# Performance work log

Measured on AMD Instinct MI355X. Metric: run time of the kernel, lower is better.

## Reference

```python
import jax, jax.numpy as jnp
import numpy as np

B, S, DM, H = 4, 4096, 1024, 16
HD = DM // H

def setup_inputs() -> dict:
    key = jax.random.key(0)
    ks = jax.random.split(key, 9)
    sc = 1.0 / np.sqrt(DM)
    return {
        "x": jax.random.normal(ks[0], (B, S, DM), dtype=jnp.float32),
        "Wq": jax.random.normal(ks[1], (DM, DM), dtype=jnp.float32) * sc,
        "bq": jnp.zeros((DM,), dtype=jnp.float32),
        "Wk": jax.random.normal(ks[2], (DM, DM), dtype=jnp.float32) * sc,
        "bk": jnp.zeros((DM,), dtype=jnp.float32),
        "Wv": jax.random.normal(ks[3], (DM, DM), dtype=jnp.float32) * sc,
        "bv": jnp.zeros((DM,), dtype=jnp.float32),
        "Wo": jax.random.normal(ks[4], (DM, DM), dtype=jnp.float32) * sc,
        "bo": jnp.zeros((DM,), dtype=jnp.float32),
    }

def _heads(t):
    # [B,S,DM] -> [B,H,S,HD]
    return t.reshape(B, S, H, HD).transpose(0, 2, 1, 3)

def reference(x, Wq, bq, Wk, bk, Wv, bv, Wo, bo):
    q = _heads(x @ Wq.T + bq)
    k = _heads(x @ Wk.T + bk)
    v = _heads(x @ Wv.T + bv)
    q = jax.nn.elu(q) + 1.0  # positive feature map
    k = jax.nn.elu(k) + 1.0
    # kv aggregation: [B,H,HD,HD]
    kv = jnp.einsum('bhsd,bhse->bhde', k, v)
    qkv = jnp.einsum('bhsd,bhde->bhse', q, kv)  # [B,H,S,HD]
    k_sum = k.sum(axis=2)  # [B,H,HD]
    normalizer = jnp.einsum('bhsd,bhd->bhs', q, k_sum) + 1e-6
    out = qkv / normalizer[..., None]
    out = out.transpose(0, 2, 1, 3).reshape(B, S, DM)
    return out @ Wo.T + bo  # dropout is identity in eval
```

## Files before the change

### kernel.cpp

```cpp
#include <hip/hip_runtime.h>
#include <math.h>

#define NROWS  16384
#define DMODEL 1024
#define NHEAD  16
#define HDIM   64
#define SEQ    4096
#define NBATCH 4
#define NBH    64
#define SCHUNK 16
#define M1     1048576u

typedef __attribute__((ext_vector_type(8))) short bf16x8;
typedef __attribute__((ext_vector_type(4))) float f32x4;

__device__ __forceinline__ unsigned short f2bf(float f) {
    unsigned u = __float_as_uint(f);
    u += 0x7FFFu + ((u >> 16) & 1u);
    return (unsigned short)(u >> 16);
}
__device__ __forceinline__ float bf2f(unsigned short h) {
    return __uint_as_float((unsigned)h << 16);
}

__device__ __forceinline__ void gload16(const void* g, void* l) {
    __builtin_amdgcn_global_load_lds(
        (const __attribute__((address_space(1))) unsigned int*)g,
        (__attribute__((address_space(3))) unsigned int*)l, 16, 0, 0);
}

__global__ __launch_bounds__(256)
void split_pair(const float* __restrict__ a, unsigned short* __restrict__ hi,
                unsigned short* __restrict__ lo, int n4)
{
    int i = blockIdx.x * 256 + threadIdx.x;
    const int stride = gridDim.x * 256;
    for (; i < n4; i += stride) {
        const float4 v = ((const float4*)a)[i];
        ushort4 H, L;
        H.x = f2bf(v.x); L.x = f2bf(v.x - bf2f(H.x));
        H.y = f2bf(v.y); L.y = f2bf(v.y - bf2f(H.y));
        H.z = f2bf(v.z); L.z = f2bf(v.z - bf2f(H.z));
        H.w = f2bf(v.w); L.w = f2bf(v.w - bf2f(H.w));
        ((ushort4*)hi)[i] = H;
        ((ushort4*)lo)[i] = L;
    }
}

__global__ __launch_bounds__(256)
void split_w4(const float* __restrict__ a0, const float* __restrict__ a1,
              const float* __restrict__ a2, const float* __restrict__ a3,
              unsigned short* __restrict__ dst)
{
    const int y = blockIdx.y;
    const float* src = (y == 0) ? a0 : (y == 1) ? a1 : (y == 2) ? a2 : a3;
    unsigned short* hi = dst + (size_t)y * 2u * M1;
    unsigned short* lo = hi + M1;
    const int i = blockIdx.x * 256 + threadIdx.x;
    const float4 v = ((const float4*)src)[i];
    ushort4 H, L;
    H.x = f2bf(v.x); L.x = f2bf(v.x - bf2f(H.x));
    H.y = f2bf(v.y); L.y = f2bf(v.y - bf2f(H.y));
    H.z = f2bf(v.z); L.z = f2bf(v.z - bf2f(H.z));
    H.w = f2bf(v.w); L.w = f2bf(v.w - bf2f(H.w));
    ((ushort4*)hi)[i] = H;
    ((ushort4*)lo)[i] = L;
}

template<int ELU>
__global__ __launch_bounds__(256)
void gemm_split(const unsigned short* __restrict__ Ah, const unsigned short* __restrict__ Al,
                const unsigned short* __restrict__ Wh, const unsigned short* __restrict__ Wl,
                const float* __restrict__ bias, float* __restrict__ C)
{
    __shared__ unsigned short lds[4 * 4096];
    const int t    = threadIdx.x;
    const int lane = t & 63;
    const int w    = t >> 6;
    const int wr   = w >> 1;
    const int wc   = w & 1;
    const int m0   = blockIdx.x * 128;
    const int n0   = blockIdx.y * 128;
    const int srow = lane >> 2;
    const int scol = (lane & 3) * 8;
    const int fr   = lane & 15;
    const int kq   = (lane >> 4) * 8;

    f32x4 acc[4][4];
#pragma unroll
    for (int i = 0; i < 4; ++i)
#pragma unroll
        for (int j = 0; j < 4; ++j)
#pragma unroll
            for (int e = 0; e < 4; ++e) acc[i][j][e] = 0.f;

    for (int k0 = 0; k0 < DMODEL; k0 += 32) {
#pragma unroll
        for (int c = 0; c < 2; ++c) {
            const int rr = (c * 4 + w) * 16 + srow;
            const size_t goffA = (size_t)(m0 + rr) * DMODEL + k0 + scol;
            const size_t goffB = (size_t)(n0 + rr) * DMODEL + k0 + scol;
            unsigned short* lbase = (unsigned short*)lds + (c * 4 + w) * 512;
            gload16(Ah + goffA, lbase);
            gload16(Al + goffA, lbase + 4096);
            gload16(Wh + goffB, lbase + 8192);
            gload16(Wl + goffB, lbase + 12288);
        }
        __syncthreads();

        bf16x8 ah[4], al[4], bh[4], bl[4];
#pragma unroll
        for (int i = 0; i < 4; ++i) {
            const int ar = wr * 64 + i * 16 + fr;
            const int br = wc * 64 + i * 16 + fr;
            ah[i] = *(const bf16x8*)&lds[ar * 32 + kq];
            al[i] = *(const bf16x8*)&lds[4096 + ar * 32 + kq];
            bh[i] = *(const bf16x8*)&lds[8192 + br * 32 + kq];
            bl[i] = *(const bf16x8*)&lds[12288 + br * 32 + kq];
        }
#pragma unroll
        for (int i = 0; i < 4; ++i)
#pragma unroll
            for (int j = 0; j < 4; ++j) {
                acc[i][j] = __builtin_amdgcn_mfma_f32_16x16x32_bf16(ah[i], bh[j], acc[i][j], 0, 0, 0);
                acc[i][j] = __builtin_amdgcn_mfma_f32_16x16x32_bf16(ah[i], bl[j], acc[i][j], 0, 0, 0);
                acc[i][j] = __builtin_amdgcn_mfma_f32_16x16x32_bf16(al[i], bh[j], acc[i][j], 0, 0, 0);
            }
        __syncthreads();
    }

    const int crow0 = m0 + wr * 64 + (lane >> 4) * 4;
    const int ccol0 = n0 + wc * 64 + fr;
#pragma unroll
    for (int j = 0; j < 4; ++j) {
        const int col = ccol0 + j * 16;
        const float bv = bias[col];
#pragma unroll
        for (int i = 0; i < 4; ++i) {
            const int row = crow0 + i * 16;
#pragma unroll
            for (int r = 0; r < 4; ++r) {
                float v = acc[i][j][r] + bv;
                if (ELU) v = (v > 0.f) ? (v + 1.f) : __expf(v);
                C[(size_t)(row + r) * DMODEL + col] = v;
            }
        }
    }
}

__global__ __launch_bounds__(512)
void kv_partial(const float* __restrict__ k, const float* __restrict__ v,
                float* __restrict__ kvp, float* __restrict__ ksp)
{
    __shared__ float Ks[32][64];
    __shared__ float Vs[32][64];
    const int t  = threadIdx.x;
    const int bh = blockIdx.x;
    const int b  = bh >> 4;
    const int h  = bh & 15;
    const int sc = blockIdx.y;
    const int d  = t & 63;
    const int e0 = (t >> 6) * 8;

    float acc[8];
#pragma unroll
    for (int j = 0; j < 8; ++j) acc[j] = 0.f;
    float ks = 0.f;

    const size_t rowbase = (size_t)b * SEQ;
    const int sbeg = sc * (SEQ / SCHUNK);
    const int send = sbeg + (SEQ / SCHUNK);
    const int lrow = t >> 4;
    const int lc4  = (t & 15) * 4;

    for (int s0 = sbeg; s0 < send; s0 += 32) {
        const size_t g = (rowbase + s0 + lrow) * DMODEL + h * HDIM + lc4;
        *(float4*)&Ks[lrow][lc4] = *(const float4*)&k[g];
        *(float4*)&Vs[lrow][lc4] = *(const float4*)&v[g];
        __syncthreads();
#pragma unroll 8
        for (int sp = 0; sp < 32; ++sp) {
            const float kd = Ks[sp][d];
            if (t < 64) ks += Ks[sp][t];
            const float4 v0 = *(const float4*)&Vs[sp][e0 + 0];
            const float4 v1 = *(const float4*)&Vs[sp][e0 + 4];
            acc[0] = fmaf(kd, v0.x, acc[0]);  acc[1] = fmaf(kd, v0.y, acc[1]);
            acc[2] = fmaf(kd, v0.z, acc[2]);  acc[3] = fmaf(kd, v0.w, acc[3]);
            acc[4] = fmaf(kd, v1.x, acc[4]);  acc[5] = fmaf(kd, v1.y, acc[5]);
            acc[6] = fmaf(kd, v1.z, acc[6]);  acc[7] = fmaf(kd, v1.w, acc[7]);
        }
        __syncthreads();
    }

    const size_t base = ((size_t)sc * NBH + bh) * HDIM;
    float4 o0; o0.x = acc[0]; o0.y = acc[1]; o0.z = acc[2]; o0.w = acc[3];
    float4 o1; o1.x = acc[4]; o1.y = acc[5]; o1.z = acc[6]; o1.w = acc[7];
    *(float4*)&kvp[(base + d) * HDIM + e0 + 0] = o0;
    *(float4*)&kvp[(base + d) * HDIM + e0 + 4] = o1;
    if (t < 64) ksp[base + t] = ks;
}

__global__ __launch_bounds__(256)
void kv_reduce(const float* __restrict__ kvp, const float* __restrict__ ksp,
               float* __restrict__ kv, float* __restrict__ ksum)
{
    const int i = blockIdx.x * 256 + threadIdx.x;
    const int NKV = NBH * HDIM * HDIM;
    if (i < NKV) {
        float s = 0.f;
#pragma unroll
        for (int c = 0; c < SCHUNK; ++c) s += kvp[(size_t)c * NKV + i];
        kv[i] = s;
    }
    if (i < NBH * HDIM) {
        float s = 0.f;
#pragma unroll
        for (int c = 0; c < SCHUNK; ++c) s += ksp[(size_t)c * NBH * HDIM + i];
        ksum[i] = s;
    }
}

__global__ __launch_bounds__(256)
void qkv_norm(const float* __restrict__ q, const float* __restrict__ kv,
              const float* __restrict__ ksum,
              unsigned short* __restrict__ ah, unsigned short* __restrict__ al)
{
    __shared__ float Qs[64][68];
    __shared__ float KVs[64][64];
    __shared__ float kss[64];
    const int t  = threadIdx.x;
    const int s0 = blockIdx.x * 64;
    const int b  = blockIdx.y;
    const int h  = blockIdx.z;
    const int bh = b * NHEAD + h;

#pragma unroll
    for (int i = 0; i < 4; ++i) {
        const int idx = i * 256 + t;
        const int row = idx >> 4;
        const int c4  = (idx & 15) * 4;
        const float4 vq = *(const float4*)&q[((size_t)b * SEQ + s0 + row) * DMODEL + h * HDIM + c4];
        *(float4*)&Qs[row][c4] = vq;
        *(float4*)&((float*)KVs)[idx * 4] = *(const float4*)&kv[(size_t)bh * HDIM * HDIM + idx * 4];
    }
    if (t < 64) kss[t] = ksum[(size_t)bh * HDIM + t];
    __syncthreads();

    const int r  = t >> 2;
    const int e0 = (t & 3) * 16;
    float out[16];
#pragma unroll
    for (int j = 0; j < 16; ++j) out[j] = 0.f;
    float nrm = 0.f;

#pragma unroll 8
    for (int d = 0; d < 64; ++d) {
        const float qd = Qs[r][d];
        nrm = fmaf(qd, kss[d], nrm);
        const float4 k0 = *(const float4*)&KVs[d][e0 + 0];
        const float4 k1 = *(const float4*)&KVs[d][e0 + 4];
        const float4 k2 = *(const float4*)&KVs[d][e0 + 8];
        const float4 k3 = *(const float4*)&KVs[d][e0 + 12];
        out[0]  = fmaf(qd, k0.x, out[0]);  out[1]  = fmaf(qd, k0.y, out[1]);
        out[2]  = fmaf(qd, k0.z, out[2]);  out[3]  = fmaf(qd, k0.w, out[3]);
        out[4]  = fmaf(qd, k1.x, out[4]);  out[5]  = fmaf(qd, k1.y, out[5]);
        out[6]  = fmaf(qd, k1.z, out[6]);  out[7]  = fmaf(qd, k1.w, out[7]);
        out[8]  = fmaf(qd, k2.x, out[8]);  out[9]  = fmaf(qd, k2.y, out[9]);
        out[10] = fmaf(qd, k2.z, out[10]); out[11] = fmaf(qd, k2.w, out[11]);
        out[12] = fmaf(qd, k3.x, out[12]); out[13] = fmaf(qd, k3.y, out[13]);
        out[14] = fmaf(qd, k3.z, out[14]); out[15] = fmaf(qd, k3.w, out[15]);
    }

    const float inv = 1.f / (nrm + 1e-6f);
    const size_t gbase = ((size_t)b * SEQ + s0 + r) * DMODEL + h * HDIM + e0;
#pragma unroll
    for (int g4 = 0; g4 < 4; ++g4) {
        ushort4 H, L;
        const float v0 = out[g4*4+0] * inv;
        const float v1 = out[g4*4+1] * inv;
        const float v2 = out[g4*4+2] * inv;
        const float v3 = out[g4*4+3] * inv;
        H.x = f2bf(v0); L.x = f2bf(v0 - bf2f(H.x));
        H.y = f2bf(v1); L.y = f2bf(v1 - bf2f(H.y));
        H.z = f2bf(v2); L.z = f2bf(v2 - bf2f(H.z));
        H.w = f2bf(v3); L.w = f2bf(v3 - bf2f(H.w));
        *(ushort4*)&ah[gbase + g4 * 4] = H;
        *(ushort4*)&al[gbase + g4 * 4] = L;
    }
}

extern "C" void kernel_launch(void* const* d_in, const int* in_sizes, int n_in,
                              void* d_out, int out_size, void* d_ws, size_t ws_size,
                              hipStream_t stream)
{
    const float* x  = (const float*)d_in[0];
    const float* Wq = (const float*)d_in[1];
    const float* bq = (const float*)d_in[2];
    const float* Wk = (const float*)d_in[3];
    const float* bk = (const float*)d_in[4];
    const float* Wv = (const float*)d_in[5];
    const float* bv = (const float*)d_in[6];
    const float* Wo = (const float*)d_in[7];
    const float* bo = (const float*)d_in[8];

    unsigned short* xh = (unsigned short*)d_ws;
    unsigned short* xl = xh + (size_t)NROWS * DMODEL;
    unsigned short* wsp = xl + (size_t)NROWS * DMODEL;
    float* buf0 = (float*)(wsp + 8u * M1);
    float* kv   = buf0 + (size_t)NROWS * DMODEL;
    float* ksum = kv + NBH * HDIM * HDIM;
    float* kvp  = ksum + NBH * HDIM;
    float* ksp  = kvp + (size_t)SCHUNK * NBH * HDIM * HDIM;
    float* vbuf = (float*)d_out;

    const dim3 gg(NROWS / 128, DMODEL / 128);
    const int n4x = NROWS * DMODEL / 4;

    split_w4<<<dim3(1024, 4), 256, 0, stream>>>(Wq, Wk, Wv, Wo, wsp);
    split_pair<<<4096, 256, 0, stream>>>(x, xh, xl, n4x);
    gemm_split<1><<<gg, 256, 0, stream>>>(xh, xl, wsp + 2u * M1, wsp + 3u * M1, bk, buf0);
    gemm_split<0><<<gg, 256, 0, stream>>>(xh, xl, wsp + 4u * M1, wsp + 5u * M1, bv, vbuf);
    kv_partial<<<dim3(NBH, SCHUNK), 512, 0, stream>>>(buf0, vbuf, kvp, ksp);
    kv_reduce<<<1024, 256, 0, stream>>>(kvp, ksp, kv, ksum);
    gemm_split<1><<<gg, 256, 0, stream>>>(xh, xl, wsp, wsp + M1, bq, buf0);
    qkv_norm<<<dim3(SEQ / 64, NBATCH, NHEAD), 256, 0, stream>>>(buf0, kv, ksum, xh, xl);
    gemm_split<0><<<gg, 256, 0, stream>>>(xh, xl, wsp + 6u * M1, wsp + 7u * M1, bo, (float*)d_out);
}
```

Before: 582.1 us.

## Use 256x256 double-buffered split-bf16 GEMM with 8 waves and block swizzle

Replaces the 128x128 single-buffered split-bf16 GEMM with a 256x256-tile, 512-thread kernel. Each block keeps two LDS stages so global loads for the next K step overlap MFMA work on the current one, and the stage loads are interleaved per A-phase with s_barrier and setprio hints. A block-index swizzle groups blocks that share A rows to improve L2 reuse. The larger tile doubles per-wave accumulators (128 fp32 regs), which raises register pressure and gives only 256 blocks, which may leave CUs underfilled.

```diff
diff --git a/kernel.cpp b/kernel.cpp
--- a/kernel.cpp
+++ b/kernel.cpp
@@ -68,75 +68,100 @@
 }
 
 template<int ELU>
-__global__ __launch_bounds__(256)
-void gemm_split(const unsigned short* __restrict__ Ah, const unsigned short* __restrict__ Al,
-                const unsigned short* __restrict__ Wh, const unsigned short* __restrict__ Wl,
-                const float* __restrict__ bias, float* __restrict__ C)
-{
-    __shared__ unsigned short lds[4 * 4096];
+__global__ __launch_bounds__(512)
+void gemm_split8(const unsigned short* __restrict__ Ah, const unsigned short* __restrict__ Al,
+                 const unsigned short* __restrict__ Wh, const unsigned short* __restrict__ Wl,
+                 const float* __restrict__ bias, float* __restrict__ C)
+{
+    __shared__ unsigned short lds[2 * 32768];
     const int t    = threadIdx.x;
     const int lane = t & 63;
-    const int w    = t >> 6;
-    const int wr   = w >> 1;
-    const int wc   = w & 1;
-    const int m0   = blockIdx.x * 128;
-    const int n0   = blockIdx.y * 128;
+    const int wv   = t >> 6;
+    const int wr   = wv >> 2;
+    const int wcn  = wv & 3;
+
+    const int bid  = blockIdx.x;
+    const int swz  = ((bid & 7) << 5) | (bid >> 3);
+    const int am0  = (swz >> 2) * 256;
+    const int bn0  = (swz & 3) * 256;
+
     const int srow = lane >> 2;
     const int scol = (lane & 3) * 8;
     const int fr   = lane & 15;
-    const int kq   = (lane >> 4) * 8;
-
-    f32x4 acc[4][4];
-#pragma unroll
-    for (int i = 0; i < 4; ++i)
+    const int j0   = lane >> 4;
+
+    f32x4 acc[8][4];
+#pragma unroll
+    for (int i = 0; i < 8; ++i)
 #pragma unroll
         for (int j = 0; j < 4; ++j)
 #pragma unroll
             for (int e = 0; e < 4; ++e) acc[i][j][e] = 0.f;
 
-    for (int k0 = 0; k0 < DMODEL; k0 += 32) {
+    auto stage = [&](int ph, int k0, unsigned wb) {
+        const unsigned short* gs = (ph == 0) ? Ah : (ph == 1) ? Al : (ph == 2) ? Wh : Wl;
+        const int rbase = (ph < 2) ? am0 : bn0;
 #pragma unroll
         for (int c = 0; c < 2; ++c) {
-            const int rr = (c * 4 + w) * 16 + srow;
-            const size_t goffA = (size_t)(m0 + rr) * DMODEL + k0 + scol;
-            const size_t goffB = (size_t)(n0 + rr) * DMODEL + k0 + scol;
-            unsigned short* lbase = (unsigned short*)lds + (c * 4 + w) * 512;
-            gload16(Ah + goffA, lbase);
-            gload16(Al + goffA, lbase + 4096);
-            gload16(Wh + goffB, lbase + 8192);
-            gload16(Wl + goffB, lbase + 12288);
+            const int grow = rbase + c * 128 + wv * 16 + srow;
+            gload16(gs + (size_t)grow * DMODEL + k0 + scol,
+                    (unsigned short*)&lds[wb + (unsigned)ph * 8192u + (unsigned)(c * 128 + wv * 16) * 32u]);
+        }
+    };
+
+#pragma unroll
+    for (int ph = 0; ph < 4; ++ph) stage(ph, 0, 0u);
+    __syncthreads();
+
+    for (int ks = 0; ks < 32; ++ks) {
+        const unsigned rb = (ks & 1) ? 32768u : 0u;
+        const unsigned wb = rb ^ 32768u;
+        const int k0n = (ks + 1) * 32;
+        const bool pf = (ks < 31);
+
+        bf16x8 bh[4], bl[4];
+#pragma unroll
+        for (int ph = 0; ph < 4; ++ph) {
+            if (ph == 0) {
+#pragma unroll
+                for (int j = 0; j < 4; ++j) {
+                    const unsigned ro = (unsigned)(wcn * 64 + j * 16 + fr) * 32u + (unsigned)j0 * 8u;
+                    bh[j] = *(const bf16x8*)&lds[rb + 16384u + ro];
+                    bl[j] = *(const bf16x8*)&lds[rb + 24576u + ro];
+                }
+            }
+            bf16x8 a_h[2], a_l[2];
+#pragma unroll
+            for (int i2 = 0; i2 < 2; ++i2) {
+                const unsigned ro = (unsigned)(wr * 128 + (ph * 2 + i2) * 16 + fr) * 32u + (unsigned)j0 * 8u;
+                a_h[i2] = *(const bf16x8*)&lds[rb + ro];
+                a_l[i2] = *(const bf16x8*)&lds[rb + 8192u + ro];
+            }
+            if (pf) stage(ph, k0n, wb);
+            __builtin_amdgcn_s_barrier();
+            __builtin_amdgcn_s_setprio(1);
+#pragma unroll
+            for (int i2 = 0; i2 < 2; ++i2)
+#pragma unroll
+                for (int j = 0; j < 4; ++j) {
+                    acc[ph * 2 + i2][j] = __builtin_amdgcn_mfma_f32_16x16x32_bf16(a_h[i2], bh[j], acc[ph * 2 + i2][j], 0, 0, 0);
+                    acc[ph * 2 + i2][j] = __builtin_amdgcn_mfma_f32_16x16x32_bf16(a_h[i2], bl[j], acc[ph * 2 + i2][j], 0, 0, 0);
+                    acc[ph * 2 + i2][j] = __builtin_amdgcn_mfma_f32_16x16x32_bf16(a_l[i2], bh[j], acc[ph * 2 + i2][j], 0, 0, 0);
+                }
+            __builtin_amdgcn_s_setprio(0);
+            if (ph < 3) __builtin_amdgcn_s_barrier();
         }
         __syncthreads();
-
-        bf16x8 ah[4], al[4], bh[4], bl[4];
-#pragma unroll
-        for (int i = 0; i < 4; ++i) {
-            const int ar = wr * 64 + i * 16 + fr;
-            const int br = wc * 64 + i * 16 + fr;
-            ah[i] = *(const bf16x8*)&lds[ar * 32 + kq];
-            al[i] = *(const bf16x8*)&lds[4096 + ar * 32 + kq];
-            bh[i] = *(const bf16x8*)&lds[8192 + br * 32 + kq];
-            bl[i] = *(const bf16x8*)&lds[12288 + br * 32 + kq];
-        }
-#pragma unroll
-        for (int i = 0; i < 4; ++i)
-#pragma unroll
-            for (int j = 0; j < 4; ++j) {
-                acc[i][j] = __builtin_amdgcn_mfma_f32_16x16x32_bf16(ah[i], bh[j], acc[i][j], 0, 0, 0);
-                acc[i][j] = __builtin_amdgcn_mfma_f32_16x16x32_bf16(ah[i], bl[j], acc[i][j], 0, 0, 0);
-                acc[i][j] = __builtin_amdgcn_mfma_f32_16x16x32_bf16(al[i], bh[j], acc[i][j], 0, 0, 0);
-            }
-        __syncthreads();
-    }
-
-    const int crow0 = m0 + wr * 64 + (lane >> 4) * 4;
-    const int ccol0 = n0 + wc * 64 + fr;
+    }
+
+    const int crow0 = am0 + wr * 128 + (lane >> 4) * 4;
+    const int ccol0 = bn0 + wcn * 64 + fr;
 #pragma unroll
     for (int j = 0; j < 4; ++j) {
         const int col = ccol0 + j * 16;
         const float bv = bias[col];
 #pragma unroll
-        for (int i = 0; i < 4; ++i) {
+        for (int i = 0; i < 8; ++i) {
             const int row = crow0 + i * 16;
 #pragma unroll
             for (int r = 0; r < 4; ++r) {
@@ -313,16 +338,16 @@
     float* ksp  = kvp + (size_t)SCHUNK * NBH * HDIM * HDIM;
     float* vbuf = (float*)d_out;
 
-    const dim3 gg(NROWS / 128, DMODEL / 128);
+    const dim3 gg(256);
     const int n4x = NROWS * DMODEL / 4;
 
     split_w4<<<dim3(1024, 4), 256, 0, stream>>>(Wq, Wk, Wv, Wo, wsp);
     split_pair<<<4096, 256, 0, stream>>>(x, xh, xl, n4x);
-    gemm_split<1><<<gg, 256, 0, stream>>>(xh, xl, wsp + 2u * M1, wsp + 3u * M1, bk, buf0);
-    gemm_split<0><<<gg, 256, 0, stream>>>(xh, xl, wsp + 4u * M1, wsp + 5u * M1, bv, vbuf);
+    gemm_split8<1><<<gg, 512, 0, stream>>>(xh, xl, wsp + 2u * M1, wsp + 3u * M1, bk, buf0);
+    gemm_split8<0><<<gg, 512, 0, stream>>>(xh, xl, wsp + 4u * M1, wsp + 5u * M1, bv, vbuf);
     kv_partial<<<dim3(NBH, SCHUNK), 512, 0, stream>>>(buf0, vbuf, kvp, ksp);
     kv_reduce<<<1024, 256, 0, stream>>>(kvp, ksp, kv, ksum);
-    gemm_split<1><<<gg, 256, 0, stream>>>(xh, xl, wsp, wsp + M1, bq, buf0);
+    gemm_split8<1><<<gg, 512, 0, stream>>>(xh, xl, wsp, wsp + M1, bq, buf0);
     qkv_norm<<<dim3(SEQ / 64, NBATCH, NHEAD), 256, 0, stream>>>(buf0, kv, ksum, xh, xl);
-    gemm_split<0><<<gg, 256, 0, stream>>>(xh, xl, wsp + 6u * M1, wsp + 7u * M1, bo, (float*)d_out);
-}
+    gemm_split8<0><<<gg, 512, 0, stream>>>(xh, xl, wsp + 6u * M1, wsp + 7u * M1, bo, (float*)d_out);
+}
```

New measurement: 485.5 us. 16.6% less time.
